# Optimization experiments

Measured on AMD Instinct MI355X. Metric: run time of the kernel, lower is better.

## Reference

```python
import jax, jax.numpy as jnp
import numpy as np
from jax import lax

SMOOTH = 1e-06
THRESH_WIDTH = 10


def _max_pool3(x):
    # 3x3 max pool, stride 1, padding 1 (torch pads with -inf for max pool)
    return lax.reduce_window(x, -jnp.inf, lax.max,
                             (1, 1, 3, 3), (1, 1, 1, 1),
                             [(0, 0), (0, 0), (1, 1), (1, 1)])


def soft_skeletonize(x):
    def body(x, _):
        min_pool = -_max_pool3(-x)
        contour = jax.nn.relu(_max_pool3(min_pool) - min_pool)
        return jax.nn.relu(x - contour), None
    x, _ = lax.scan(body, x, None, length=THRESH_WIDTH)
    return x


def norm_intersection(center_line, vessel):
    smooth = 1.0
    b, c = center_line.shape[:2]
    clf = center_line.reshape(b, c, -1)
    vf = vessel.reshape(b, c, -1)
    intersection = (clf * vf).sum(-1)
    return (intersection + smooth) / (clf.sum(-1) + smooth)


def dice_loss(pred, target):
    intersection = (pred * target).sum()
    denominator = pred.sum() + target.sum()
    dice_score = (2.0 * intersection + SMOOTH) / (denominator + SMOOTH)
    return 1.0 - dice_score


def soft_cldice_loss(pred, target):
    cl_pred = soft_skeletonize(pred)
    target_skeleton = soft_skeletonize(target)
    iflat = norm_intersection(cl_pred, target)
    tflat = norm_intersection(target_skeleton, pred)
    intersection = (iflat * tflat).sum()
    return 1.0 - 2.0 * intersection / (iflat + tflat).sum()


def setup_inputs() -> dict:
    key = jax.random.key(0)
    k1, k2 = jax.random.split(key)
    shape = (64, 1, 512, 512)
    pred = jax.random.uniform(k1, shape, dtype=jnp.float32)
    target = jax.random.uniform(k2, shape, dtype=jnp.float32)
    return {"pred": pred, "target": target}


def reference(pred, target):
    return 0.8 * dice_loss(pred, target) + 0.2 * soft_cldice_loss(pred, target)
```

## Files before the change

### kernel.cpp

```cpp
#include <hip/hip_runtime.h>


#define H 512
#define W 512
#define NIMG 64
#define TOT 128
#define IMG_ELEMS (H * W)
#define RSTRIPS 32
#define SROWS (H / RSTRIPS)
#define NDICE_SLOTS 64

__device__ float g_A[(size_t)TOT * IMG_ELEMS];
__device__ float g_B[(size_t)TOT * IMG_ELEMS];
__device__ float g_acc[NIMG * 4];
__device__ float g_dice[NDICE_SLOTS * 16];

#define SEL_A 2
#define SEL_B 3

struct F8 { float4 a, b; };

__device__ __forceinline__ F8 f8fill(float v) {
  F8 r; r.a = make_float4(v, v, v, v); r.b = r.a; return r;
}
__device__ __forceinline__ F8 f8min(const F8& x, const F8& y) {
  F8 r;
  r.a.x = fminf(x.a.x, y.a.x); r.a.y = fminf(x.a.y, y.a.y);
  r.a.z = fminf(x.a.z, y.a.z); r.a.w = fminf(x.a.w, y.a.w);
  r.b.x = fminf(x.b.x, y.b.x); r.b.y = fminf(x.b.y, y.b.y);
  r.b.z = fminf(x.b.z, y.b.z); r.b.w = fminf(x.b.w, y.b.w);
  return r;
}
__device__ __forceinline__ F8 f8max(const F8& x, const F8& y) {
  F8 r;
  r.a.x = fmaxf(x.a.x, y.a.x); r.a.y = fmaxf(x.a.y, y.a.y);
  r.a.z = fmaxf(x.a.z, y.a.z); r.a.w = fmaxf(x.a.w, y.a.w);
  r.b.x = fmaxf(x.b.x, y.b.x); r.b.y = fmaxf(x.b.y, y.b.y);
  r.b.z = fmaxf(x.b.z, y.b.z); r.b.w = fmaxf(x.b.w, y.b.w);
  return r;
}
__device__ __forceinline__ F8 ero8(const F8& v, int lane) {
  float L = __shfl_up(v.b.w, 1, 64);
  if (lane == 0) L = __builtin_inff();
  float R = __shfl_down(v.a.x, 1, 64);
  if (lane == 63) R = __builtin_inff();
  F8 e;
  e.a.x = fminf(L,     fminf(v.a.x, v.a.y));
  e.a.y = fminf(v.a.x, fminf(v.a.y, v.a.z));
  e.a.z = fminf(v.a.y, fminf(v.a.z, v.a.w));
  e.a.w = fminf(v.a.z, fminf(v.a.w, v.b.x));
  e.b.x = fminf(v.a.w, fminf(v.b.x, v.b.y));
  e.b.y = fminf(v.b.x, fminf(v.b.y, v.b.z));
  e.b.z = fminf(v.b.y, fminf(v.b.z, v.b.w));
  e.b.w = fminf(v.b.z, fminf(v.b.w, R));
  return e;
}
__device__ __forceinline__ F8 dil8(const F8& v, int lane) {
  float L = __shfl_up(v.b.w, 1, 64);
  if (lane == 0) L = -__builtin_inff();
  float R = __shfl_down(v.a.x, 1, 64);
  if (lane == 63) R = -__builtin_inff();
  F8 d;
  d.a.x = fmaxf(L,     fmaxf(v.a.x, v.a.y));
  d.a.y = fmaxf(v.a.x, fmaxf(v.a.y, v.a.z));
  d.a.z = fmaxf(v.a.y, fmaxf(v.a.z, v.a.w));
  d.a.w = fmaxf(v.a.z, fmaxf(v.a.w, v.b.x));
  d.b.x = fmaxf(v.a.w, fmaxf(v.b.x, v.b.y));
  d.b.y = fmaxf(v.b.x, fmaxf(v.b.y, v.b.z));
  d.b.z = fmaxf(v.b.y, fmaxf(v.b.z, v.b.w));
  d.b.w = fmaxf(v.b.z, fmaxf(v.b.w, R));
  return d;
}
__device__ __forceinline__ F8 f8relu_sub(const F8& x, const F8& y) {
  F8 r;
  r.a.x = fmaxf(x.a.x - y.a.x, 0.f); r.a.y = fmaxf(x.a.y - y.a.y, 0.f);
  r.a.z = fmaxf(x.a.z - y.a.z, 0.f); r.a.w = fmaxf(x.a.w - y.a.w, 0.f);
  r.b.x = fmaxf(x.b.x - y.b.x, 0.f); r.b.y = fmaxf(x.b.y - y.b.y, 0.f);
  r.b.z = fmaxf(x.b.z - y.b.z, 0.f); r.b.w = fmaxf(x.b.w - y.b.w, 0.f);
  return r;
}
__device__ __forceinline__ float f8dot(const F8& x, const float4& oa,
                                       const float4& ob) {
  return x.a.x * oa.x + x.a.y * oa.y + x.a.z * oa.z + x.a.w * oa.w
       + x.b.x * ob.x + x.b.y * ob.y + x.b.z * ob.z + x.b.w * ob.w;
}
__device__ __forceinline__ float f8sum(const F8& x) {
  return x.a.x + x.a.y + x.a.z + x.a.w + x.b.x + x.b.y + x.b.z + x.b.w;
}

template <int MODE>
__device__ __forceinline__ void skel2_core(
    const float* __restrict__ simg, float* __restrict__ dimg,
    const float* __restrict__ oimg, bool isPred, int r0, int lane,
    float out3[3]) {
  const float PINF = __builtin_inff();
  float a0 = 0.f, a1 = 0.f, a2 = 0.f;

  auto loadrow = [&](int r) -> F8 {
    F8 v;
    if (r >= 0 && r < H) {
      const float4* rp = (const float4*)(simg + (size_t)r * W);
      v.a = rp[lane * 2];
      v.b = rp[lane * 2 + 1];
    } else {
      v = f8fill(PINF);
    }
    return v;
  };

  float4 tca = make_float4(0.f, 0.f, 0.f, 0.f), tcb = tca;
  float4 tna = tca, tnb = tca;

  int s = r0 - 2;
  F8 xa  = loadrow(s - 2);
  F8 xb  = loadrow(s - 1);
  F8 xc  = loadrow(s);
  F8 xp  = loadrow(s + 1);
  F8 xn  = loadrow(s + 2);
  F8 xn2 = loadrow(s + 3);
  F8 em = ero8(f8min(xa, f8min(xb, xc)), lane);
  if (s - 1 < 0) em = f8fill(-PINF);
  F8 ec = ero8(f8min(xb, f8min(xc, xp)), lane);
  if (s < 0) ec = f8fill(-PINF);
  F8 pmaxA = f8max(em, ec);
  F8 pminA = f8min(xc, xp);

  auto step1 = [&]() -> F8 {
    F8 ep = ero8(f8min(pminA, xn), lane);
    if (s + 1 < 0 || s + 1 >= H) ep = f8fill(-PINF);
    F8 dil = dil8(f8max(pmaxA, ep), lane);
    F8 y = f8relu_sub(xc, f8relu_sub(dil, ec));
    if (s < 0 || s >= H) y = f8fill(PINF);

    if (MODE == 1 && s >= r0 && s < r0 + SROWS) {
      if (isPred) {
        a0 += f8dot(xc, tca, tcb);
        a1 += f8sum(xc);
      } else {
        a2 += f8sum(xc);
      }
    }

    pminA = f8min(xp, xn);
    pmaxA = f8max(ec, ep);
    xc = xp; xp = xn; xn = xn2; xn2 = loadrow(s + 4);

    if (MODE == 1) {
      tca = tna; tcb = tnb;
      const int rt = s + 2;
      if (isPred && rt >= r0 && rt < r0 + SROWS) {
        const float4* tp = (const float4*)(oimg + (size_t)rt * W);
        tna = tp[lane * 2];
        tnb = tp[lane * 2 + 1];
      }
    }

    ec = ep;
    ++s;
    return y;
  };

  F8 ya = step1();
  F8 yb = step1();
  F8 yc = step1();
  F8 yp = step1();
  F8 yn = step1();
  F8 e2m = ero8(f8min(ya, f8min(yb, yc)), lane);
  if (r0 - 1 < 0) e2m = f8fill(-PINF);
  F8 e2c = ero8(f8min(yb, f8min(yc, yp)), lane);
  F8 pmax2 = f8max(e2m, e2c);
  F8 pmin2 = f8min(yc, yp);

  float4 oa = make_float4(0.f, 0.f, 0.f, 0.f), ob = oa;
  if (MODE == 2) {
    const float4* orp = (const float4*)(oimg + (size_t)r0 * W);
    oa = orp[lane * 2];
    ob = orp[lane * 2 + 1];
  }

  #pragma unroll 2
  for (int t = r0; t < r0 + SROWS; ++t) {
    F8 ynew = step1();

    float4 na, nb;
    if (MODE == 2) {
      const int tn_ = (t + 1 < r0 + SROWS) ? t + 1 : t;
      const float4* orp = (const float4*)(oimg + (size_t)tn_ * W);
      na = orp[lane * 2];
      nb = orp[lane * 2 + 1];
    }

    F8 e2p = ero8(f8min(pmin2, yn), lane);
    if (t + 1 >= H) e2p = f8fill(-PINF);
    F8 d2 = dil8(f8max(pmax2, e2p), lane);
    F8 z = f8relu_sub(yc, f8relu_sub(d2, e2c));

    if (MODE == 2) {
      a0 += f8dot(z, oa, ob);
      a1 += f8sum(z);
      oa = na; ob = nb;
    } else {
      float4* op = (float4*)(dimg + (size_t)t * W);
      op[lane * 2]     = z.a;
      op[lane * 2 + 1] = z.b;
    }
    pmin2 = f8min(yp, yn);
    pmax2 = f8max(e2c, e2p);
    yc = yp; yp = yn; yn = ynew; e2c = e2p;
  }

  if (MODE != 0) {
    #pragma unroll
    for (int o = 32; o; o >>= 1) {
      a0 += __shfl_down(a0, o, 64);
      a1 += __shfl_down(a1, o, 64);
      if (MODE == 1) a2 += __shfl_down(a2, o, 64);
    }
    out3[0] = a0; out3[1] = a1; out3[2] = a2;
  }
}

__global__ __launch_bounds__(256) void pass_start(
    const float* __restrict__ pred, const float* __restrict__ target) {
  const int wid  = blockIdx.x * 4 + (threadIdx.x >> 6);
  const int lane = threadIdx.x & 63;
  const int u    = wid / RSTRIPS;
  const int r0   = (wid % RSTRIPS) * SROWS;
  const bool isPred = (u < NIMG);
  const float* src = isPred ? pred + (size_t)u * IMG_ELEMS
                            : target + (size_t)(u - NIMG) * IMG_ELEMS;
  const float* o = isPred ? target + (size_t)u * IMG_ELEMS : nullptr;
  float* dst = (float*)g_A + (size_t)u * IMG_ELEMS;

  float out3[3] = {0.f, 0.f, 0.f};
  skel2_core<1>(src, dst, o, isPred, r0, lane, out3);

  __shared__ float red[4][3];
  const int wave = threadIdx.x >> 6;
  if (lane == 0) {
    red[wave][0] = out3[0]; red[wave][1] = out3[1]; red[wave][2] = out3[2];
  }
  __syncthreads();
  if (threadIdx.x < 3) {
    float sv = red[0][threadIdx.x] + red[1][threadIdx.x] +
               red[2][threadIdx.x] + red[3][threadIdx.x];
    atomicAdd(&g_dice[(blockIdx.x & (NDICE_SLOTS - 1)) * 16 + threadIdx.x], sv);
  }
}

__global__ __launch_bounds__(256) void pass_plain(int srcSel) {
  const float* src = (srcSel == SEL_A) ? (const float*)g_A : (const float*)g_B;
  float* dst = (srcSel == SEL_A) ? g_B : g_A;
  const int wid  = blockIdx.x * 4 + (threadIdx.x >> 6);
  const int lane = threadIdx.x & 63;
  const int u    = wid / RSTRIPS;
  const int r0   = (wid % RSTRIPS) * SROWS;
  skel2_core<0>(src + (size_t)u * IMG_ELEMS, dst + (size_t)u * IMG_ELEMS,
                nullptr, false, r0, lane, nullptr);
}

__global__ __launch_bounds__(256) void pass_reduce(
    const float* __restrict__ pred, const float* __restrict__ target) {
  const int wid  = blockIdx.x * 4 + (threadIdx.x >> 6);
  const int lane = threadIdx.x & 63;
  const int u    = wid / RSTRIPS;
  const int r0   = (wid % RSTRIPS) * SROWS;
  const bool isPred = (u < NIMG);
  const int img = isPred ? u : u - NIMG;
  const int accBase = isPred ? 0 : 2;
  const float* src = (const float*)g_B + (size_t)u * IMG_ELEMS;
  const float* o = isPred ? target + (size_t)img * IMG_ELEMS
                          : pred + (size_t)img * IMG_ELEMS;

  float out3[3] = {0.f, 0.f, 0.f};
  skel2_core<2>(src, nullptr, o, isPred, r0, lane, out3);

  __shared__ float red[4][2];
  const int wave = threadIdx.x >> 6;
  if (lane == 0) { red[wave][0] = out3[0]; red[wave][1] = out3[1]; }
  __syncthreads();
  if (threadIdx.x < 2) {
    float sv = red[0][threadIdx.x] + red[1][threadIdx.x] +
               red[2][threadIdx.x] + red[3][threadIdx.x];
    atomicAdd(&g_acc[img * 4 + accBase + threadIdx.x], sv);
  }
}

__global__ void zero_acc() {
  for (int i = threadIdx.x; i < NIMG * 4; i += 256) g_acc[i] = 0.0f;
  for (int i = threadIdx.x; i < NDICE_SLOTS * 16; i += 256) g_dice[i] = 0.0f;
}

__global__ void final_kernel(float* __restrict__ out) {
  const int lane = threadIdx.x;
  float s1 = g_acc[lane * 4 + 0], s2 = g_acc[lane * 4 + 1];
  float s3 = g_acc[lane * 4 + 2], s4 = g_acc[lane * 4 + 3];
  float iflat = (s1 + 1.0f) / (s2 + 1.0f);
  float tflat = (s3 + 1.0f) / (s4 + 1.0f);
  float prod = iflat * tflat;
  float ssum = iflat + tflat;
  float d0 = g_dice[lane * 16 + 0];
  float d1 = g_dice[lane * 16 + 1];
  float d2 = g_dice[lane * 16 + 2];
  #pragma unroll
  for (int o = 32; o; o >>= 1) {
    prod += __shfl_down(prod, o, 64);
    ssum += __shfl_down(ssum, o, 64);
    d0   += __shfl_down(d0, o, 64);
    d1   += __shfl_down(d1, o, 64);
    d2   += __shfl_down(d2, o, 64);
  }
  if (lane == 0) {
    float cldice = 1.0f - 2.0f * prod / ssum;
    float dice = 1.0f - (2.0f * d0 + 1e-6f) / (d1 + d2 + 1e-6f);
    out[0] = 0.8f * dice + 0.2f * cldice;
  }
}

extern "C" void kernel_launch(void* const* d_in, const int* in_sizes, int n_in,
                              void* d_out, int out_size, void* d_ws, size_t ws_size,
                              hipStream_t stream) {
  const float* pred   = (const float*)d_in[0];
  const float* target = (const float*)d_in[1];
  float* out = (float*)d_out;
  (void)d_ws; (void)ws_size;

  const int nblocks = TOT * RSTRIPS / 4;

  zero_acc<<<1, 256, 0, stream>>>();
  pass_start<<<nblocks, 256, 0, stream>>>(pred, target);
  pass_plain<<<nblocks, 256, 0, stream>>>(SEL_A);
  pass_plain<<<nblocks, 256, 0, stream>>>(SEL_B);
  pass_plain<<<nblocks, 256, 0, stream>>>(SEL_A);
  pass_reduce<<<nblocks, 256, 0, stream>>>(pred, target);
  final_kernel<<<1, 64, 0, stream>>>(out);
}
```

Before: 429.6 us.

## Stream source rows through per-wave LDS ring via async global_load_lds

```diff
diff --git a/kernel.cpp b/kernel.cpp
--- a/kernel.cpp
+++ b/kernel.cpp
@@ -71,6 +71,14 @@
   d.b.w = fmaxf(v.b.z, fmaxf(v.b.w, R));
   return d;
 }
+__device__ __forceinline__ F8 f8sub(const F8& x, const F8& y) {
+  F8 r;
+  r.a.x = x.a.x - y.a.x; r.a.y = x.a.y - y.a.y;
+  r.a.z = x.a.z - y.a.z; r.a.w = x.a.w - y.a.w;
+  r.b.x = x.b.x - y.b.x; r.b.y = x.b.y - y.b.y;
+  r.b.z = x.b.z - y.b.z; r.b.w = x.b.w - y.b.w;
+  return r;
+}
 __device__ __forceinline__ F8 f8relu_sub(const F8& x, const F8& y) {
   F8 r;
   r.a.x = fmaxf(x.a.x - y.a.x, 0.f); r.a.y = fmaxf(x.a.y - y.a.y, 0.f);
@@ -88,23 +96,42 @@
   return x.a.x + x.a.y + x.a.z + x.a.w + x.b.x + x.b.y + x.b.z + x.b.w;
 }
 
+__device__ __forceinline__ void gload_lds16(const float* g, float* l) {
+  __builtin_amdgcn_global_load_lds(
+      (const __attribute__((address_space(1))) void*)g,
+      (__attribute__((address_space(3))) void*)l, 16, 0, 0);
+}
+
+#define WAITV(N)                                                   \
+  do {                                                             \
+    asm volatile("s_waitcnt vmcnt(" #N ")" ::: "memory");          \
+    __builtin_amdgcn_sched_barrier(0);                             \
+  } while (0)
+
 template <int MODE>
 __device__ __forceinline__ void skel2_core(
     const float* __restrict__ simg, float* __restrict__ dimg,
     const float* __restrict__ oimg, bool isPred, int r0, int lane,
-    float out3[3]) {
+    float* __restrict__ ringw, float out3[3]) {
   const float PINF = __builtin_inff();
   float a0 = 0.f, a1 = 0.f, a2 = 0.f;
-
-  auto loadrow = [&](int r) -> F8 {
+  int slot_c = 0, slot_i = 0;
+
+  auto issue = [&](int r) {
+    int rc = r < 0 ? 0 : (r > H - 1 ? H - 1 : r);
+    const float* gp = simg + (size_t)rc * W + (lane << 2);
+    float* lp = ringw + slot_i * 512;
+    gload_lds16(gp, lp);
+    gload_lds16(gp + 256, lp + 256);
+    slot_i = (slot_i == 3) ? 0 : slot_i + 1;
+  };
+  auto consume = [&](int r) -> F8 {
     F8 v;
-    if (r >= 0 && r < H) {
-      const float4* rp = (const float4*)(simg + (size_t)r * W);
-      v.a = rp[lane * 2];
-      v.b = rp[lane * 2 + 1];
-    } else {
-      v = f8fill(PINF);
-    }
+    const float4* lp4 = (const float4*)(ringw + slot_c * 512);
+    v.a = lp4[lane * 2];
+    v.b = lp4[lane * 2 + 1];
+    if (r < 0 || r >= H) v = f8fill(PINF);
+    slot_c = (slot_c == 3) ? 0 : slot_c + 1;
     return v;
   };
 
@@ -112,12 +139,13 @@
   float4 tna = tca, tnb = tca;
 
   int s = r0 - 2;
-  F8 xa  = loadrow(s - 2);
-  F8 xb  = loadrow(s - 1);
-  F8 xc  = loadrow(s);
-  F8 xp  = loadrow(s + 1);
-  F8 xn  = loadrow(s + 2);
-  F8 xn2 = loadrow(s + 3);
+  issue(r0 - 4); issue(r0 - 3); issue(r0 - 2);
+  WAITV(4); F8 xa = consume(r0 - 4); issue(r0 - 1);
+  WAITV(4); F8 xb = consume(r0 - 3); issue(r0);
+  WAITV(4); F8 xc = consume(r0 - 2); issue(r0 + 1);
+  WAITV(4); F8 xp = consume(r0 - 1); issue(r0 + 2);
+  WAITV(4); F8 xn = consume(r0);     issue(r0 + 3);
+
   F8 em = ero8(f8min(xa, f8min(xb, xc)), lane);
   if (s - 1 < 0) em = f8fill(-PINF);
   F8 ec = ero8(f8min(xb, f8min(xc, xp)), lane);
@@ -125,11 +153,11 @@
   F8 pmaxA = f8max(em, ec);
   F8 pminA = f8min(xc, xp);
 
-  auto step1 = [&]() -> F8 {
+  auto step1 = [&](F8 xnew) -> F8 {
     F8 ep = ero8(f8min(pminA, xn), lane);
     if (s + 1 < 0 || s + 1 >= H) ep = f8fill(-PINF);
     F8 dil = dil8(f8max(pmaxA, ep), lane);
-    F8 y = f8relu_sub(xc, f8relu_sub(dil, ec));
+    F8 y = f8relu_sub(xc, f8sub(dil, ec));
     if (s < 0 || s >= H) y = f8fill(PINF);
 
     if (MODE == 1 && s >= r0 && s < r0 + SROWS) {
@@ -143,7 +171,7 @@
 
     pminA = f8min(xp, xn);
     pmaxA = f8max(ec, ep);
-    xc = xp; xp = xn; xn = xn2; xn2 = loadrow(s + 4);
+    xc = xp; xp = xn; xn = xnew;
 
     if (MODE == 1) {
       tca = tna; tcb = tnb;
@@ -160,11 +188,13 @@
     return y;
   };
 
-  F8 ya = step1();
-  F8 yb = step1();
-  F8 yc = step1();
-  F8 yp = step1();
-  F8 yn = step1();
+  F8 ya, yb, yc, yp, yn;
+  { WAITV(4); F8 xw = consume(s + 3); issue(s + 6); ya = step1(xw); }
+  { WAITV(4); F8 xw = consume(s + 3); issue(s + 6); yb = step1(xw); }
+  { WAITV(4); F8 xw = consume(s + 3); issue(s + 6); yc = step1(xw); }
+  { WAITV(4); F8 xw = consume(s + 3); issue(s + 6); yp = step1(xw); }
+  { WAITV(4); F8 xw = consume(s + 3); issue(s + 6); yn = step1(xw); }
+
   F8 e2m = ero8(f8min(ya, f8min(yb, yc)), lane);
   if (r0 - 1 < 0) e2m = f8fill(-PINF);
   F8 e2c = ero8(f8min(yb, f8min(yc, yp)), lane);
@@ -178,9 +208,10 @@
     ob = orp[lane * 2 + 1];
   }
 
-  #pragma unroll 2
-  for (int t = r0; t < r0 + SROWS; ++t) {
-    F8 ynew = step1();
+  auto body = [&](int t) {
+    F8 xw = consume(t + 6);
+    issue(t + 9);
+    F8 ynew = step1(xw);
 
     float4 na, nb;
     if (MODE == 2) {
@@ -193,7 +224,7 @@
     F8 e2p = ero8(f8min(pmin2, yn), lane);
     if (t + 1 >= H) e2p = f8fill(-PINF);
     F8 d2 = dil8(f8max(pmax2, e2p), lane);
-    F8 z = f8relu_sub(yc, f8relu_sub(d2, e2c));
+    F8 z = f8relu_sub(yc, f8sub(d2, e2c));
 
     if (MODE == 2) {
       a0 += f8dot(z, oa, ob);
@@ -207,6 +238,16 @@
     pmin2 = f8min(yp, yn);
     pmax2 = f8max(e2c, e2p);
     yc = yp; yp = yn; yn = ynew; e2c = e2p;
+  };
+
+  int t = r0;
+  { WAITV(4); body(t); ++t; }
+  { WAITV(6); body(t); ++t; }
+  { WAITV(8); body(t); ++t; }
+  for (; t < r0 + SROWS; ++t) {
+    if (MODE == 1 && isPred) { WAITV(16); }
+    else                     { WAITV(10); }
+    body(t);
   }
 
   if (MODE != 0) {
@@ -222,6 +263,7 @@
 
 __global__ __launch_bounds__(256) void pass_start(
     const float* __restrict__ pred, const float* __restrict__ target) {
+  __shared__ float ring[4][4][512];
   const int wid  = blockIdx.x * 4 + (threadIdx.x >> 6);
   const int lane = threadIdx.x & 63;
   const int u    = wid / RSTRIPS;
@@ -233,7 +275,8 @@
   float* dst = (float*)g_A + (size_t)u * IMG_ELEMS;
 
   float out3[3] = {0.f, 0.f, 0.f};
-  skel2_core<1>(src, dst, o, isPred, r0, lane, out3);
+  skel2_core<1>(src, dst, o, isPred, r0, lane, &ring[threadIdx.x >> 6][0][0],
+                out3);
 
   __shared__ float red[4][3];
   const int wave = threadIdx.x >> 6;
@@ -249,6 +292,7 @@
 }
 
 __global__ __launch_bounds__(256) void pass_plain(int srcSel) {
+  __shared__ float ring[4][4][512];
   const float* src = (srcSel == SEL_A) ? (const float*)g_A : (const float*)g_B;
   float* dst = (srcSel == SEL_A) ? g_B : g_A;
   const int wid  = blockIdx.x * 4 + (threadIdx.x >> 6);
@@ -256,11 +300,13 @@
   const int u    = wid / RSTRIPS;
   const int r0   = (wid % RSTRIPS) * SROWS;
   skel2_core<0>(src + (size_t)u * IMG_ELEMS, dst + (size_t)u * IMG_ELEMS,
-                nullptr, false, r0, lane, nullptr);
+                nullptr, false, r0, lane, &ring[threadIdx.x >> 6][0][0],
+                nullptr);
 }
 
 __global__ __launch_bounds__(256) void pass_reduce(
     const float* __restrict__ pred, const float* __restrict__ target) {
+  __shared__ float ring[4][4][512];
   const int wid  = blockIdx.x * 4 + (threadIdx.x >> 6);
   const int lane = threadIdx.x & 63;
   const int u    = wid / RSTRIPS;
@@ -273,7 +319,8 @@
                           : pred + (size_t)img * IMG_ELEMS;
 
   float out3[3] = {0.f, 0.f, 0.f};
-  skel2_core<2>(src, nullptr, o, isPred, r0, lane, out3);
+  skel2_core<2>(src, nullptr, o, isPred, r0, lane,
+                &ring[threadIdx.x >> 6][0][0], out3);
 
   __shared__ float red[4][2];
   const int wave = threadIdx.x >> 6;
```

After: 459.1 us. 6.9% more time.
